# Performance work log

Measured on AMD Instinct MI355X. Metric: run time of the kernel, lower is better.

Reference implementation:

```python
import jax, jax.numpy as jnp
import numpy as np

NEG = -9e15

def setup_inputs() -> dict:
    key = jax.random.key(0)
    k1, k2, k3, k4, k5, k6 = jax.random.split(key, 6)
    N, Fin, Fout = 8192, 256, 128
    inp = jax.random.normal(k1, (N, Fin), dtype=jnp.float32)
    adj = jax.random.randint(k2, (N, N), 0, 2, dtype=jnp.int32)
    W_w = jax.random.normal(k3, (Fout, Fin), dtype=jnp.float32) / np.sqrt(Fin)
    W_b = jax.random.normal(k4, (Fout,), dtype=jnp.float32) * 0.01
    a_w = jax.random.normal(k5, (1, 2 * Fout), dtype=jnp.float32) / np.sqrt(2 * Fout)
    a_b = jax.random.normal(k6, (1,), dtype=jnp.float32) * 0.01
    return {"input": inp, "adj": adj, "W_w": W_w, "W_b": W_b, "a_w": a_w, "a_b": a_b}

def reference(input, adj, W_w, W_b, a_w, a_b):
    alpha = 0.2
    Fout = W_w.shape[0]
    h = input @ W_w.T + W_b                      # [N, Fout]
    # a([h_i || h_j]) = a1.h_i + a2.h_j + b  (exact decomposition of concat+linear)
    a1 = a_w[0, :Fout]
    a2 = a_w[0, Fout:]
    e = jax.nn.leaky_relu((h @ a1)[:, None] + (h @ a2)[None, :] + a_b[0],
                          negative_slope=alpha)   # [N, N]
    scores = jnp.where(adj > 0, e, NEG)
    attention = jax.nn.softmax(scores, axis=1)    # dropout in eval mode = identity
    h_prime = attention @ h                       # [N, Fout]
    return jax.nn.elu(h_prime)
```

## Files before the change

### kernel.cpp

```cpp
#include <hip/hip_runtime.h>
#include <hip/hip_bf16.h>
#include <cmath>

#define NN 8192
#define FIN 256
#define FOUT 128
#define ROWS 32
#define JWIN 64

typedef short short8 __attribute__((ext_vector_type(8)));
typedef float f32x16 __attribute__((ext_vector_type(16)));

static __device__ __forceinline__ unsigned short f2bf(float f) {
    unsigned u = __float_as_uint(f);
    u += 0x7fffu + ((u >> 16) & 1u);
    return (unsigned short)(u >> 16);
}

__global__ __launch_bounds__(256, 2)
void gat_pass_a(const float* __restrict__ input, const float* __restrict__ W,
                const float* __restrict__ Wb, const float* __restrict__ aw,
                const float* __restrict__ ab, unsigned short* __restrict__ hT2,
                float* __restrict__ s_out, float* __restrict__ t_out) {
    const int tid = threadIdx.x;
    const int w = tid >> 6, l = tid & 63;
    const int l5 = l >> 5, l31 = l & 31;
    const int nt = w >> 1, mh = w & 1;
    const int bx = blockIdx.x;
    const int i = bx * 64 + nt * 32 + l31;

    f32x16 acc0 = {}; f32x16 acc1 = {};
    #pragma unroll
    for (int ks = 0; ks < FIN / 16; ++ks) {
        const int c0 = ks * 16 + l5 * 8;
        const float4 b0 = *(const float4*)(input + (size_t)i * FIN + c0);
        const float4 b1 = *(const float4*)(input + (size_t)i * FIN + c0 + 4);
        short8 bf;
        bf[0]=(short)f2bf(b0.x); bf[1]=(short)f2bf(b0.y); bf[2]=(short)f2bf(b0.z); bf[3]=(short)f2bf(b0.w);
        bf[4]=(short)f2bf(b1.x); bf[5]=(short)f2bf(b1.y); bf[6]=(short)f2bf(b1.z); bf[7]=(short)f2bf(b1.w);
        {
            const int kcol = l31 + 32 * (2 * mh + 0);
            const float4 a0 = *(const float4*)(W + (size_t)kcol * FIN + c0);
            const float4 a1 = *(const float4*)(W + (size_t)kcol * FIN + c0 + 4);
            short8 af;
            af[0]=(short)f2bf(a0.x); af[1]=(short)f2bf(a0.y); af[2]=(short)f2bf(a0.z); af[3]=(short)f2bf(a0.w);
            af[4]=(short)f2bf(a1.x); af[5]=(short)f2bf(a1.y); af[6]=(short)f2bf(a1.z); af[7]=(short)f2bf(a1.w);
            acc0 = __builtin_amdgcn_mfma_f32_32x32x16_bf16(af, bf, acc0, 0, 0, 0);
        }
        {
            const int kcol = l31 + 32 * (2 * mh + 1);
            const float4 a0 = *(const float4*)(W + (size_t)kcol * FIN + c0);
            const float4 a1 = *(const float4*)(W + (size_t)kcol * FIN + c0 + 4);
            short8 af;
            af[0]=(short)f2bf(a0.x); af[1]=(short)f2bf(a0.y); af[2]=(short)f2bf(a0.z); af[3]=(short)f2bf(a0.w);
            af[4]=(short)f2bf(a1.x); af[5]=(short)f2bf(a1.y); af[6]=(short)f2bf(a1.z); af[7]=(short)f2bf(a1.w);
            acc1 = __builtin_amdgcn_mfma_f32_32x32x16_bf16(af, bf, acc1, 0, 0, 0);
        }
    }
    __shared__ float sred[4][32];
    __shared__ float tred[4][32];
    float sacc = 0.f, tacc = 0.f;
    #pragma unroll
    for (int m = 0; m < 2; ++m) {
        #pragma unroll
        for (int r = 0; r < 16; ++r) {
            const int kcol = 32 * (2 * mh + m) + 4 * l5 + (r & 3) + 8 * (r >> 2);
            const float hv = (m ? acc1[r] : acc0[r]) + Wb[kcol];
            hT2[((size_t)bx * FOUT + kcol) * 64 + (nt * 32 + l31)] = f2bf(hv);
            sacc += hv * aw[kcol];
            tacc += hv * aw[FOUT + kcol];
        }
    }
    sacc += __shfl_xor(sacc, 32);
    tacc += __shfl_xor(tacc, 32);
    if (l < 32) { sred[w][l] = sacc; tred[w][l] = tacc; }
    __syncthreads();
    if (mh == 0 && l < 32) {
        s_out[i] = sred[w][l] + sred[w + 1][l];
        t_out[i] = tred[w][l] + tred[w + 1][l] + ab[0];
    }
}

__global__ __launch_bounds__(256, 4)
void gat_pass_b(const int* __restrict__ adj, const unsigned short* __restrict__ hT2,
                const float* __restrict__ s_in, const float* __restrict__ t_in,
                float* __restrict__ numw, float* __restrict__ dpart, int jc) {
    __shared__ float red[FOUT * ROWS];
    __shared__ float denb[4][ROWS];
    __shared__ unsigned long long mbuf[2][ROWS];
    const int tid = threadIdx.x;
    const int wv = tid >> 6, l = tid & 63;
    const int l5 = l >> 5, l31 = l & 31;
    const int i0 = blockIdx.x * ROWS;
    const int chunk = blockIdx.y;
    const int jb = chunk * jc;
    const int nwin = jc / JWIN;
    const float si = s_in[i0 + l31];

    const int* abase = adj + (size_t)(i0 + wv * 8 + (l >> 4)) * NN + (l & 15) * 4;

    f32x16 acc0 = {}, acc1 = {}, acc2 = {}, acc3 = {};
    float dacc = 0.f;

    auto packq = [&](const int4& a, int q, unsigned long long* mb) {
        const unsigned long long b0 = __ballot(a.x > 0);
        const unsigned long long b1 = __ballot(a.y > 0);
        const unsigned long long b2 = __ballot(a.z > 0);
        const unsigned long long b3 = __ballot(a.w > 0);
        const int k = l & 3;
        const int sh = 16 * k;
        if ((l >> 2) == q) {
            const unsigned long long v = ((b0 >> sh) & 0xFFFFull)
                                       | (((b1 >> sh) & 0xFFFFull) << 16)
                                       | (((b2 >> sh) & 0xFFFFull) << 32)
                                       | (((b3 >> sh) & 0xFFFFull) << 48);
            mb[wv * 8 + q * 4 + k] = v;
        }
    };

    int4 R0 = *(const int4*)(abase + jb);
    int4 R1 = *(const int4*)(abase + 4 * NN + jb);
    packq(R0, 0, mbuf[0]);
    packq(R1, 1, mbuf[0]);

    const int bitb = wv * 4 + l5 * 2;

    for (int w = 0; w < nwin; ++w) {
        const int jw = jb + w * JWIN;
        __syncthreads();
        const unsigned long long m = mbuf[w & 1][l31] >> bitb;
        const int j0 = jw + wv * 16;
        const float4 t0 = *(const float4*)(t_in + j0 + l5 * 8);
        const float4 t1 = *(const float4*)(t_in + j0 + l5 * 8 + 4);
        const unsigned short* fbp = hT2 + ((size_t)(jw >> 6) * FOUT + l31) * 64 + wv * 16 + l5 * 8;
        const short8 af0 = *(const short8*)(fbp);
        const short8 af1 = *(const short8*)(fbp + 2048);
        const short8 af2 = *(const short8*)(fbp + 4096);
        const short8 af3 = *(const short8*)(fbp + 6144);
        if (w + 1 < nwin) {
            R0 = *(const int4*)(abase + jw + JWIN);
            R1 = *(const int4*)(abase + 4 * NN + jw + JWIN);
        }
        short8 bf;
        float x, p;
        x = si + t0.x; x = fmaxf(x, 0.2f * x); p = __expf(x);
        p = ((m >> 0)  & 1ull) ? p : 0.f; dacc += p; bf[0] = (short)f2bf(p);
        x = si + t0.y; x = fmaxf(x, 0.2f * x); p = __expf(x);
        p = ((m >> 16) & 1ull) ? p : 0.f; dacc += p; bf[1] = (short)f2bf(p);
        x = si + t0.z; x = fmaxf(x, 0.2f * x); p = __expf(x);
        p = ((m >> 32) & 1ull) ? p : 0.f; dacc += p; bf[2] = (short)f2bf(p);
        x = si + t0.w; x = fmaxf(x, 0.2f * x); p = __expf(x);
        p = ((m >> 48) & 1ull) ? p : 0.f; dacc += p; bf[3] = (short)f2bf(p);
        x = si + t1.x; x = fmaxf(x, 0.2f * x); p = __expf(x);
        p = ((m >> 1)  & 1ull) ? p : 0.f; dacc += p; bf[4] = (short)f2bf(p);
        x = si + t1.y; x = fmaxf(x, 0.2f * x); p = __expf(x);
        p = ((m >> 17) & 1ull) ? p : 0.f; dacc += p; bf[5] = (short)f2bf(p);
        x = si + t1.z; x = fmaxf(x, 0.2f * x); p = __expf(x);
        p = ((m >> 33) & 1ull) ? p : 0.f; dacc += p; bf[6] = (short)f2bf(p);
        x = si + t1.w; x = fmaxf(x, 0.2f * x); p = __expf(x);
        p = ((m >> 49) & 1ull) ? p : 0.f; dacc += p; bf[7] = (short)f2bf(p);

        acc0 = __builtin_amdgcn_mfma_f32_32x32x16_bf16(af0, bf, acc0, 0, 0, 0);
        acc1 = __builtin_amdgcn_mfma_f32_32x32x16_bf16(af1, bf, acc1, 0, 0, 0);
        acc2 = __builtin_amdgcn_mfma_f32_32x32x16_bf16(af2, bf, acc2, 0, 0, 0);
        acc3 = __builtin_amdgcn_mfma_f32_32x32x16_bf16(af3, bf, acc3, 0, 0, 0);

        if (w + 1 < nwin) {
            unsigned long long* mb = mbuf[(w + 1) & 1];
            packq(R0, 0, mb);
            packq(R1, 1, mb);
        }
    }

    #pragma unroll
    for (int ph = 0; ph < 4; ++ph) {
        __syncthreads();
        if (wv == ph) {
            #pragma unroll
            for (int r = 0; r < 16; ++r) {
                const int fr = (r & 3) + 8 * (r >> 2) + 4 * l5;
                if (ph == 0) {
                    red[(fr     ) * ROWS + l31] = acc0[r];
                    red[(fr + 32) * ROWS + l31] = acc1[r];
                    red[(fr + 64) * ROWS + l31] = acc2[r];
                    red[(fr + 96) * ROWS + l31] = acc3[r];
                } else {
                    red[(fr     ) * ROWS + l31] += acc0[r];
                    red[(fr + 32) * ROWS + l31] += acc1[r];
                    red[(fr + 64) * ROWS + l31] += acc2[r];
                    red[(fr + 96) * ROWS + l31] += acc3[r];
                }
            }
        }
    }
    dacc += __shfl_xor(dacc, 32);
    if (l5 == 0) denb[wv][l31] = dacc;
    __syncthreads();

    #pragma unroll
    for (int e = 0; e < 4; ++e) {
        const int f = e * 32 + (tid >> 3);
        const int io = (tid & 7) * 4;
        *(float4*)(numw + ((size_t)chunk * FOUT + f) * NN + i0 + io) =
            *(const float4*)(red + f * ROWS + io);
    }
    if (tid < ROWS)
        dpart[(size_t)chunk * NN + i0 + tid] =
            denb[0][tid] + denb[1][tid] + denb[2][tid] + denb[3][tid];
}

__global__ __launch_bounds__(256)
void gat_reduce(const float* __restrict__ numw, const float* __restrict__ dpart,
                float* __restrict__ out, int nchunk) {
    __shared__ float tile[FOUT * 33];
    __shared__ float dent[32];
    const int t = threadIdx.x;
    const int i0 = blockIdx.x * 32;
    if (t < 32) {
        float d = 0.f;
        for (int c = 0; c < nchunk; ++c) d += dpart[(size_t)c * NN + i0 + t];
        dent[t] = d;
    }
    __syncthreads();
    #pragma unroll
    for (int e = 0; e < 4; ++e) {
        const int f = e * 32 + (t >> 3);
        const int io = (t & 7) * 4;
        float4 s = {0.f, 0.f, 0.f, 0.f};
        for (int c = 0; c < nchunk; ++c) {
            const float4 v = *(const float4*)(numw + ((size_t)c * FOUT + f) * NN + i0 + io);
            s.x += v.x; s.y += v.y; s.z += v.z; s.w += v.w;
        }
        float v;
        v = s.x / dent[io + 0]; tile[f * 33 + io + 0] = (v > 0.f) ? v : expm1f(v);
        v = s.y / dent[io + 1]; tile[f * 33 + io + 1] = (v > 0.f) ? v : expm1f(v);
        v = s.z / dent[io + 2]; tile[f * 33 + io + 2] = (v > 0.f) ? v : expm1f(v);
        v = s.w / dent[io + 3]; tile[f * 33 + io + 3] = (v > 0.f) ? v : expm1f(v);
    }
    __syncthreads();
    #pragma unroll
    for (int e = 0; e < 4; ++e) {
        const int row = (t >> 5) * 4 + e;
        const int fo = (t & 31) * 4;
        const float4 v = { tile[(fo + 0) * 33 + row], tile[(fo + 1) * 33 + row],
                           tile[(fo + 2) * 33 + row], tile[(fo + 3) * 33 + row] };
        *(float4*)(out + (size_t)(i0 + row) * FOUT + fo) = v;
    }
}

extern "C" void kernel_launch(void* const* d_in, const int* in_sizes, int n_in,
                              void* d_out, int out_size, void* d_ws, size_t ws_size,
                              hipStream_t stream) {
    const float* input = (const float*)d_in[0];
    const int*   adj   = (const int*)d_in[1];
    const float* Ww    = (const float*)d_in[2];
    const float* Wb    = (const float*)d_in[3];
    const float* aw    = (const float*)d_in[4];
    const float* ab    = (const float*)d_in[5];
    float* out = (float*)d_out;

    char* ws = (char*)d_ws;
    unsigned short* hT2 = (unsigned short*)ws;
    float* s_buf = (float*)(ws + (size_t)FOUT * NN * 2);
    float* t_buf = s_buf + NN;

    int nchunk = 4;
    while (nchunk > 1) {
        size_t need = (size_t)FOUT * NN * 2 + 2 * (size_t)NN * 4
                    + (size_t)nchunk * NN * 4
                    + (size_t)nchunk * NN * FOUT * 4;
        if (need <= ws_size) break;
        nchunk >>= 1;
    }
    float* dpart = t_buf + NN;
    float* numw = dpart + (size_t)nchunk * NN;
    const int jc = NN / nchunk;

    gat_pass_a<<<dim3(NN / 64), 256, 0, stream>>>(input, Ww, Wb, aw, ab, hT2, s_buf, t_buf);
    gat_pass_b<<<dim3(NN / ROWS, nchunk), 256, 0, stream>>>(adj, hT2, s_buf, t_buf, numw, dpart, jc);
    gat_reduce<<<dim3(NN / 32), 256, 0, stream>>>(numw, dpart, out, nchunk);
}
```

Measured before the change: 120.4 us.

## Give each wave its own j-span in pass B and drop block barriers

Pass B is restructured so each of the 4 waves handles a separate quarter of the chunk's columns for all 32 rows. Each wave loads and packs its own adjacency mask into a private shared buffer, which replaces the per-window block-wide __syncthreads with wave barriers. The h tile is stored in an MFMA-fragment-contiguous layout (hT3) so each lane does one contiguous 16-byte load per fragment. The chunk count is now fixed at 4 rather than derived from workspace size, and occupancy is lowered to 3 blocks per CU because of the higher register use from 8 in-flight adjacency loads.

```diff
diff --git a/kernel.cpp b/kernel.cpp
--- a/kernel.cpp
+++ b/kernel.cpp
@@ -6,10 +6,14 @@
 #define FIN 256
 #define FOUT 128
 #define ROWS 32
-#define JWIN 64
+#define NCH 4
+#define JC (NN / NCH)
+#define JSPAN (JC / 4)
+#define NWIN (JSPAN / 64)
 
 typedef short short8 __attribute__((ext_vector_type(8)));
 typedef float f32x16 __attribute__((ext_vector_type(16)));
+typedef unsigned long long u64;
 
 static __device__ __forceinline__ unsigned short f2bf(float f) {
     unsigned u = __float_as_uint(f);
@@ -20,7 +24,7 @@
 __global__ __launch_bounds__(256, 2)
 void gat_pass_a(const float* __restrict__ input, const float* __restrict__ W,
                 const float* __restrict__ Wb, const float* __restrict__ aw,
-                const float* __restrict__ ab, unsigned short* __restrict__ hT2,
+                const float* __restrict__ ab, unsigned short* __restrict__ hT3,
                 float* __restrict__ s_out, float* __restrict__ t_out) {
     const int tid = threadIdx.x;
     const int w = tid >> 6, l = tid & 63;
@@ -60,13 +64,19 @@
     __shared__ float sred[4][32];
     __shared__ float tred[4][32];
     float sacc = 0.f, tacc = 0.f;
+    const int jloc = nt * 32 + l31;
+    const int ksb = jloc >> 4;
+    const int lane_j = 32 * ((jloc >> 3) & 1);
+    const int e = jloc & 7;
     #pragma unroll
     for (int m = 0; m < 2; ++m) {
         #pragma unroll
         for (int r = 0; r < 16; ++r) {
             const int kcol = 32 * (2 * mh + m) + 4 * l5 + (r & 3) + 8 * (r >> 2);
             const float hv = (m ? acc1[r] : acc0[r]) + Wb[kcol];
-            hT2[((size_t)bx * FOUT + kcol) * 64 + (nt * 32 + l31)] = f2bf(hv);
+            const int fg = kcol >> 5;
+            const int lane = (kcol & 31) + lane_j;
+            hT3[((((size_t)bx * 4 + fg) * 4 + ksb) * 64 + lane) * 8 + e] = f2bf(hv);
             sacc += hv * aw[kcol];
             tacc += hv * aw[FOUT + kcol];
         }
@@ -81,96 +91,102 @@
     }
 }
 
-__global__ __launch_bounds__(256, 4)
-void gat_pass_b(const int* __restrict__ adj, const unsigned short* __restrict__ hT2,
+__global__ __launch_bounds__(256, 3)
+void gat_pass_b(const int* __restrict__ adj, const unsigned short* __restrict__ hT3,
                 const float* __restrict__ s_in, const float* __restrict__ t_in,
-                float* __restrict__ numw, float* __restrict__ dpart, int jc) {
+                float* __restrict__ numw, float* __restrict__ dpart) {
     __shared__ float red[FOUT * ROWS];
     __shared__ float denb[4][ROWS];
-    __shared__ unsigned long long mbuf[2][ROWS];
+    __shared__ u64 mbuf[4][2][ROWS];
     const int tid = threadIdx.x;
     const int wv = tid >> 6, l = tid & 63;
     const int l5 = l >> 5, l31 = l & 31;
     const int i0 = blockIdx.x * ROWS;
     const int chunk = blockIdx.y;
-    const int jb = chunk * jc;
-    const int nwin = jc / JWIN;
+    const int jwv = chunk * JC + wv * JSPAN;
     const float si = s_in[i0 + l31];
 
-    const int* abase = adj + (size_t)(i0 + wv * 8 + (l >> 4)) * NN + (l & 15) * 4;
+    const int* ab = adj + (size_t)(i0 + (l >> 4)) * NN + (l & 15) * 4 + jwv;
+    u64* mb = &mbuf[wv][0][0];
 
     f32x16 acc0 = {}, acc1 = {}, acc2 = {}, acc3 = {};
     float dacc = 0.f;
 
-    auto packq = [&](const int4& a, int q, unsigned long long* mb) {
-        const unsigned long long b0 = __ballot(a.x > 0);
-        const unsigned long long b1 = __ballot(a.y > 0);
-        const unsigned long long b2 = __ballot(a.z > 0);
-        const unsigned long long b3 = __ballot(a.w > 0);
-        const int k = l & 3;
-        const int sh = 16 * k;
-        if ((l >> 2) == q) {
-            const unsigned long long v = ((b0 >> sh) & 0xFFFFull)
-                                       | (((b1 >> sh) & 0xFFFFull) << 16)
-                                       | (((b2 >> sh) & 0xFFFFull) << 32)
-                                       | (((b3 >> sh) & 0xFFFFull) << 48);
-            mb[wv * 8 + q * 4 + k] = v;
-        }
-    };
-
-    int4 R0 = *(const int4*)(abase + jb);
-    int4 R1 = *(const int4*)(abase + 4 * NN + jb);
-    packq(R0, 0, mbuf[0]);
-    packq(R1, 1, mbuf[0]);
-
-    const int bitb = wv * 4 + l5 * 2;
-
-    for (int w = 0; w < nwin; ++w) {
-        const int jw = jb + w * JWIN;
-        __syncthreads();
-        const unsigned long long m = mbuf[w & 1][l31] >> bitb;
-        const int j0 = jw + wv * 16;
-        const float4 t0 = *(const float4*)(t_in + j0 + l5 * 8);
-        const float4 t1 = *(const float4*)(t_in + j0 + l5 * 8 + 4);
-        const unsigned short* fbp = hT2 + ((size_t)(jw >> 6) * FOUT + l31) * 64 + wv * 16 + l5 * 8;
-        const short8 af0 = *(const short8*)(fbp);
-        const short8 af1 = *(const short8*)(fbp + 2048);
-        const short8 af2 = *(const short8*)(fbp + 4096);
-        const short8 af3 = *(const short8*)(fbp + 6144);
-        if (w + 1 < nwin) {
-            R0 = *(const int4*)(abase + jw + JWIN);
-            R1 = *(const int4*)(abase + 4 * NN + jw + JWIN);
-        }
-        short8 bf;
-        float x, p;
-        x = si + t0.x; x = fmaxf(x, 0.2f * x); p = __expf(x);
-        p = ((m >> 0)  & 1ull) ? p : 0.f; dacc += p; bf[0] = (short)f2bf(p);
-        x = si + t0.y; x = fmaxf(x, 0.2f * x); p = __expf(x);
-        p = ((m >> 16) & 1ull) ? p : 0.f; dacc += p; bf[1] = (short)f2bf(p);
-        x = si + t0.z; x = fmaxf(x, 0.2f * x); p = __expf(x);
-        p = ((m >> 32) & 1ull) ? p : 0.f; dacc += p; bf[2] = (short)f2bf(p);
-        x = si + t0.w; x = fmaxf(x, 0.2f * x); p = __expf(x);
-        p = ((m >> 48) & 1ull) ? p : 0.f; dacc += p; bf[3] = (short)f2bf(p);
-        x = si + t1.x; x = fmaxf(x, 0.2f * x); p = __expf(x);
-        p = ((m >> 1)  & 1ull) ? p : 0.f; dacc += p; bf[4] = (short)f2bf(p);
-        x = si + t1.y; x = fmaxf(x, 0.2f * x); p = __expf(x);
-        p = ((m >> 17) & 1ull) ? p : 0.f; dacc += p; bf[5] = (short)f2bf(p);
-        x = si + t1.z; x = fmaxf(x, 0.2f * x); p = __expf(x);
-        p = ((m >> 33) & 1ull) ? p : 0.f; dacc += p; bf[6] = (short)f2bf(p);
-        x = si + t1.w; x = fmaxf(x, 0.2f * x); p = __expf(x);
-        p = ((m >> 49) & 1ull) ? p : 0.f; dacc += p; bf[7] = (short)f2bf(p);
-
-        acc0 = __builtin_amdgcn_mfma_f32_32x32x16_bf16(af0, bf, acc0, 0, 0, 0);
-        acc1 = __builtin_amdgcn_mfma_f32_32x32x16_bf16(af1, bf, acc1, 0, 0, 0);
-        acc2 = __builtin_amdgcn_mfma_f32_32x32x16_bf16(af2, bf, acc2, 0, 0, 0);
-        acc3 = __builtin_amdgcn_mfma_f32_32x32x16_bf16(af3, bf, acc3, 0, 0, 0);
-
-        if (w + 1 < nwin) {
-            unsigned long long* mb = mbuf[(w + 1) & 1];
-            packq(R0, 0, mb);
-            packq(R1, 1, mb);
-        }
-    }
+    int4 R[8];
+    const int kk = l & 3;
+    const int sh = 16 * kk;
+    const int lq = l >> 2;
+
+    #define PACKQ(q, buf)                                                        \
+    {                                                                            \
+        const int4 a = R[q];                                                     \
+        const u64 b0 = __ballot(a.x > 0);                                        \
+        const u64 b1 = __ballot(a.y > 0);                                        \
+        const u64 b2 = __ballot(a.z > 0);                                        \
+        const u64 b3 = __ballot(a.w > 0);                                        \
+        const u64 v = ((b0 >> sh) & 0xFFFFull) | (((b1 >> sh) & 0xFFFFull) << 16)\
+                    | (((b2 >> sh) & 0xFFFFull) << 32)                           \
+                    | (((b3 >> sh) & 0xFFFFull) << 48);                          \
+        if (lq == (q)) mb[(buf) * ROWS + (q) * 4 + kk] = v;                      \
+    }
+
+    #pragma unroll
+    for (int q = 0; q < 8; ++q) R[q] = *(const int4*)(ab + (size_t)q * 4 * NN);
+    #pragma unroll
+    for (int q = 0; q < 8; ++q) PACKQ(q, 0)
+    __builtin_amdgcn_wave_barrier();
+
+    for (int w = 0; w < NWIN; ++w) {
+        const u64 myw = mb[(w & 1) * ROWS + l31];
+        if (w + 1 < NWIN) {
+            #pragma unroll
+            for (int q = 0; q < 8; ++q)
+                R[q] = *(const int4*)(ab + (size_t)q * 4 * NN + (w + 1) * 64);
+        }
+        const int tile = (jwv + w * 64) >> 6;
+        #pragma unroll
+        for (int ks = 0; ks < 4; ++ks) {
+            const int jsl = jwv + w * 64 + ks * 16 + l5 * 8;
+            const float4 t0 = *(const float4*)(t_in + jsl);
+            const float4 t1 = *(const float4*)(t_in + jsl + 4);
+            const u64 m = myw >> (ks * 4 + l5 * 2);
+            short8 bf;
+            float x, p;
+            x = si + t0.x; x = fmaxf(x, 0.2f * x); p = __expf(x);
+            p = ((m >> 0)  & 1ull) ? p : 0.f; dacc += p; bf[0] = (short)f2bf(p);
+            x = si + t0.y; x = fmaxf(x, 0.2f * x); p = __expf(x);
+            p = ((m >> 16) & 1ull) ? p : 0.f; dacc += p; bf[1] = (short)f2bf(p);
+            x = si + t0.z; x = fmaxf(x, 0.2f * x); p = __expf(x);
+            p = ((m >> 32) & 1ull) ? p : 0.f; dacc += p; bf[2] = (short)f2bf(p);
+            x = si + t0.w; x = fmaxf(x, 0.2f * x); p = __expf(x);
+            p = ((m >> 48) & 1ull) ? p : 0.f; dacc += p; bf[3] = (short)f2bf(p);
+            x = si + t1.x; x = fmaxf(x, 0.2f * x); p = __expf(x);
+            p = ((m >> 1)  & 1ull) ? p : 0.f; dacc += p; bf[4] = (short)f2bf(p);
+            x = si + t1.y; x = fmaxf(x, 0.2f * x); p = __expf(x);
+            p = ((m >> 17) & 1ull) ? p : 0.f; dacc += p; bf[5] = (short)f2bf(p);
+            x = si + t1.z; x = fmaxf(x, 0.2f * x); p = __expf(x);
+            p = ((m >> 33) & 1ull) ? p : 0.f; dacc += p; bf[6] = (short)f2bf(p);
+            x = si + t1.w; x = fmaxf(x, 0.2f * x); p = __expf(x);
+            p = ((m >> 49) & 1ull) ? p : 0.f; dacc += p; bf[7] = (short)f2bf(p);
+
+            const unsigned short* hp =
+                hT3 + (((size_t)tile * 4) * 4 + ks) * 512 + (size_t)l * 8;
+            const short8 af0 = *(const short8*)(hp);
+            const short8 af1 = *(const short8*)(hp + 2048);
+            const short8 af2 = *(const short8*)(hp + 4096);
+            const short8 af3 = *(const short8*)(hp + 6144);
+            acc0 = __builtin_amdgcn_mfma_f32_32x32x16_bf16(af0, bf, acc0, 0, 0, 0);
+            acc1 = __builtin_amdgcn_mfma_f32_32x32x16_bf16(af1, bf, acc1, 0, 0, 0);
+            acc2 = __builtin_amdgcn_mfma_f32_32x32x16_bf16(af2, bf, acc2, 0, 0, 0);
+            acc3 = __builtin_amdgcn_mfma_f32_32x32x16_bf16(af3, bf, acc3, 0, 0, 0);
+        }
+        if (w + 1 < NWIN) {
+            #pragma unroll
+            for (int q = 0; q < 8; ++q) PACKQ(q, (w + 1) & 1)
+        }
+        __builtin_amdgcn_wave_barrier();
+    }
+    #undef PACKQ
 
     #pragma unroll
     for (int ph = 0; ph < 4; ++ph) {
@@ -197,12 +213,12 @@
     if (l5 == 0) denb[wv][l31] = dacc;
     __syncthreads();
 
+    float* nb = numw + (size_t)chunk * FOUT * NN;
     #pragma unroll
     for (int e = 0; e < 4; ++e) {
         const int f = e * 32 + (tid >> 3);
         const int io = (tid & 7) * 4;
-        *(float4*)(numw + ((size_t)chunk * FOUT + f) * NN + i0 + io) =
-            *(const float4*)(red + f * ROWS + io);
+        *(float4*)(nb + (size_t)f * NN + i0 + io) = *(const float4*)(red + f * ROWS + io);
     }
     if (tid < ROWS)
         dpart[(size_t)chunk * NN + i0 + tid] =
@@ -260,23 +276,13 @@
     float* out = (float*)d_out;
 
     char* ws = (char*)d_ws;
-    unsigned short* hT2 = (unsigned short*)ws;
+    unsigned short* hT3 = (unsigned short*)ws;
     float* s_buf = (float*)(ws + (size_t)FOUT * NN * 2);
     float* t_buf = s_buf + NN;
-
-    int nchunk = 4;
-    while (nchunk > 1) {
-        size_t need = (size_t)FOUT * NN * 2 + 2 * (size_t)NN * 4
-                    + (size_t)nchunk * NN * 4
-                    + (size_t)nchunk * NN * FOUT * 4;
-        if (need <= ws_size) break;
-        nchunk >>= 1;
-    }
     float* dpart = t_buf + NN;
-    float* numw = dpart + (size_t)nchunk * NN;
-    const int jc = NN / nchunk;
-
-    gat_pass_a<<<dim3(NN / 64), 256, 0, stream>>>(input, Ww, Wb, aw, ab, hT2, s_buf, t_buf);
-    gat_pass_b<<<dim3(NN / ROWS, nchunk), 256, 0, stream>>>(adj, hT2, s_buf, t_buf, numw, dpart, jc);
-    gat_reduce<<<dim3(NN / 32), 256, 0, stream>>>(numw, dpart, out, nchunk);
-}
+    float* numw = dpart + (size_t)NCH * NN;
+
+    gat_pass_a<<<dim3(NN / 64), 256, 0, stream>>>(input, Ww, Wb, aw, ab, hT3, s_buf, t_buf);
+    gat_pass_b<<<dim3(NN / ROWS, NCH), 256, 0, stream>>>(adj, hT3, s_buf, t_buf, numw, dpart);
+    gat_reduce<<<dim3(NN / 32), 256, 0, stream>>>(numw, dpart, out, NCH);
+}
```

After: 115.5 us. -4.1%, faster.
